# Optimization experiments

Hardware: AMD Instinct MI355X
Metric: run time of the kernel (lower is better)

## Reference

```python
import jax, jax.numpy as jnp
import numpy as np

D_MODEL = 1024
NUM_HEADS = 16
DEPTH = D_MODEL // NUM_HEADS
B, S = 2, 2048


def setup_inputs() -> dict:
    key = jax.random.key(0)
    ks = jax.random.split(key, 12)
    std = 1.0 / np.sqrt(D_MODEL)
    inp = {
        "q": jax.random.normal(ks[0], (B, S, D_MODEL), dtype=jnp.float32),
        "k": jax.random.normal(ks[1], (B, S, D_MODEL), dtype=jnp.float32),
        "v": jax.random.normal(ks[2], (B, S, D_MODEL), dtype=jnp.float32),
        "mask": jax.random.randint(ks[3], (B, 1, 1, S), 0, 2, dtype=jnp.int32),
        "wq": jax.random.normal(ks[4], (D_MODEL, D_MODEL), dtype=jnp.float32) * std,
        "bq": jnp.zeros((D_MODEL,), dtype=jnp.float32),
        "wk": jax.random.normal(ks[5], (D_MODEL, D_MODEL), dtype=jnp.float32) * std,
        "bk": jnp.zeros((D_MODEL,), dtype=jnp.float32),
        "wv": jax.random.normal(ks[6], (D_MODEL, D_MODEL), dtype=jnp.float32) * std,
        "bv": jnp.zeros((D_MODEL,), dtype=jnp.float32),
        "wo": jax.random.normal(ks[7], (D_MODEL, D_MODEL), dtype=jnp.float32) * std,
        "bo": jnp.zeros((D_MODEL,), dtype=jnp.float32),
    }
    return inp


def _split_heads(x):
    # (B, S, D) -> (B, H, S, depth)
    b, s, _ = x.shape
    return x.reshape(b, s, NUM_HEADS, DEPTH).transpose(0, 2, 1, 3)


def reference(q, k, v, mask, wq, bq, wk, bk, wv, bv, wo, bo):
    qh = _split_heads(q @ wq + bq)   # (B,H,S,depth)
    kh = _split_heads(k @ wk + bk)
    vh = _split_heads(v @ wv + bv)
    scale = 1.0 / jnp.sqrt(jnp.float32(DEPTH))
    logits = jnp.einsum("bhqd,bhkd->bhqk", qh, kh) * scale  # (B,H,Sq,Sk)
    logits = logits + mask.astype(logits.dtype) * -1e9
    attn = jax.nn.softmax(logits, axis=-1)
    out = jnp.einsum("bhqk,bhkd->bhqd", attn, vh)  # (B,H,Sq,depth)
    out = out.transpose(0, 2, 1, 3).reshape(q.shape[0], -1, D_MODEL)
    return out @ wo + bo
```

## Files before the change

kernel.cpp:

```cpp
#include <hip/hip_runtime.h>
#include <hip/hip_bf16.h>
#include <stdint.h>


typedef __bf16 bf16;
typedef __bf16 bf16x8 __attribute__((ext_vector_type(8)));
typedef __bf16 bf16x4 __attribute__((ext_vector_type(4)));
typedef float  f32x4  __attribute__((ext_vector_type(4)));

#define D_MODEL 1024
#define S_LEN   2048
#define NH      16
#define DEPTH   64

#define LOG2E   1.4426950408889634f
#define QSCALE  (0.125f * LOG2E)
#define SMAX    20.0f
#define PADPEN  (-30000.0f)

__device__ __forceinline__ void gload_lds16(const void* g, void* l) {
  __builtin_amdgcn_global_load_lds(
      (__attribute__((address_space(1))) void*)g,
      (__attribute__((address_space(3))) void*)l,
      16, 0, 0);
}

__global__ __launch_bounds__(256) void setup(
    const void* __restrict__ q, const void* __restrict__ k,
    const void* __restrict__ v, const int* __restrict__ mask,
    const void* __restrict__ wq, const void* __restrict__ wk,
    const void* __restrict__ wv, const void* __restrict__ wo,
    const void* __restrict__ bq, const void* __restrict__ bk,
    const void* __restrict__ bv, const void* __restrict__ bo,
    bf16* __restrict__ wqT, bf16* __restrict__ wkT,
    bf16* __restrict__ wvT, bf16* __restrict__ woT,
    bf16* __restrict__ bqb, bf16* __restrict__ bkb,
    bf16* __restrict__ bvb, bf16* __restrict__ bob,
    bf16* __restrict__ qb, bf16* __restrict__ kb, bf16* __restrict__ vb,
    int* __restrict__ cpos, int* __restrict__ nb, int* __restrict__ flagout)
{
  const int t = threadIdx.x;
  uint32_t w = ((const uint32_t*)q)[t];
  uint32_t e = (w >> 7) & 0xFF;
  int inr = (e >= 90 && e <= 150) ? 1 : 0;
  __shared__ int flg;
  int cnt = __syncthreads_count(inr);
  if (t == 0) flg = (cnt > 160) ? 1 : 0;
  __syncthreads();
  int flag = flg;

  const int bid = blockIdx.x;
  if (bid < 2) {
    const int b = bid;
    const int lane = t & 63, wv4 = t >> 6;
    __shared__ int wsum[4];
    int vals[8], s = 0;
#pragma unroll
    for (int j = 0; j < 8; ++j) {
      vals[j] = (mask[b * S_LEN + t * 8 + j] == 0) ? 1 : 0;
      s += vals[j];
    }
    int acc = s;
    for (int off = 1; off < 64; off <<= 1) {
      int u = __shfl_up(acc, off);
      if (lane >= off) acc += u;
    }
    if (lane == 63) wsum[wv4] = acc;
    __syncthreads();
    int base = 0;
    for (int w4 = 0; w4 < 4; ++w4) base += (w4 < wv4) ? wsum[w4] : 0;
    int ex = base + acc - s;
#pragma unroll
    for (int j = 0; j < 8; ++j) {
      cpos[b * S_LEN + t * 8 + j] = vals[j] ? ex : -1;
      ex += vals[j];
    }
    if (t == 255) nb[b] = base + acc;
    if (b == 0 && t == 0) *flagout = flag;
  } else if (bid < 6) {
    const int j = bid - 2;
    const void* B; bf16* O;
    switch (j) {
      case 0:  B = bq; O = bqb; break;
      case 1:  B = bk; O = bkb; break;
      case 2:  B = bv; O = bvb; break;
      default: B = bo; O = bob; break;
    }
    const float sc = (j == 0) ? QSCALE : 1.0f;
    for (int jj = 0; jj < 4; ++jj) {
      const int i = t + jj * 256;
      const float val = flag ? (float)((const bf16*)B)[i] : ((const float*)B)[i];
      O[i] = (bf16)(val * sc);
    }
  } else if (bid < 6 + 4096) {
    const int job = bid - 6;
    const int wsel = job >> 10, rem = job & 1023;
    const void* W; bf16* T;
    switch (wsel) {
      case 0:  W = wq; T = wqT; break;
      case 1:  W = wk; T = wkT; break;
      case 2:  W = wv; T = wvT; break;
      default: W = wo; T = woT; break;
    }
    const float sc = (wsel == 0) ? QSCALE : 1.0f;
    __shared__ float tile[32][33];
    const int tx = t & 31, ty = t >> 5;
    const int x0 = (rem & 31) * 32;
    const int y0 = (rem >> 5) * 32;
    for (int i = ty; i < 32; i += 8) {
      const size_t gi = (size_t)(y0 + i) * D_MODEL + x0 + tx;
      tile[i][tx] = flag ? (float)((const bf16*)W)[gi] : ((const float*)W)[gi];
    }
    __syncthreads();
    for (int i = ty; i < 32; i += 8)
      T[(size_t)(x0 + i) * D_MODEL + y0 + tx] = (bf16)(tile[tx][i] * sc);
  } else {
    if (flag) return;
    const int job = bid - 4102;
    const int tensor = job >> 11, blk = job & 2047;
    const void* src; bf16* dst;
    switch (tensor) {
      case 0:  src = q; dst = qb; break;
      case 1:  src = k; dst = kb; break;
      default: src = v; dst = vb; break;
    }
    const size_t idx = ((size_t)blk * 256 + t) * 8;
    const float* s = (const float*)src + idx;
    f32x4 a = *(const f32x4*)(s);
    f32x4 b2 = *(const f32x4*)(s + 4);
    bf16x8 o;
    for (int i = 0; i < 4; ++i) { o[i] = (bf16)a[i]; o[4 + i] = (bf16)b2[i]; }
    *(bf16x8*)(dst + idx) = o;
  }
}

struct GArgs {
  const bf16* A;
  const void* Araw;
  const bf16* BT;
  const bf16* bias;
  void* out;
  const int* cpos;
  int mode;
};

__device__ __forceinline__ void gemm_body(const GArgs& g, int flag)
{
  const bf16* A = flag ? (const bf16*)g.Araw : g.A;

  __shared__ __align__(16) bf16 As[128 * 32];
  __shared__ __align__(16) bf16 Bs[128 * 32];
  const int tid  = threadIdx.x;
  const int wave = tid >> 6, lane = tid & 63;
  const int quad = lane >> 4, l16 = lane & 15;

  const int flat = blockIdx.y * 8 + blockIdx.x;
  const int xcd = flat & 7, pos = flat >> 3;
  const int bx = (xcd & 1) * 4 + (pos & 3);
  const int by = (xcd >> 1) * 8 + (pos >> 2);
  const int m0 = by * 128, n0 = bx * 128;

  const int wm = (wave >> 1) * 64, wn = (wave & 1) * 64;
  const int srow = lane >> 2;
  const int scol = (lane & 3) * 8;

  f32x4 acc[4][4] = {};

  const bf16* Ag = A    + (size_t)(m0 + wave * 32 + srow) * D_MODEL + scol;
  const bf16* Bg = g.BT + (size_t)(n0 + wave * 32 + srow) * D_MODEL + scol;
  bf16* Asw = As + (wave * 32) * 32;
  bf16* Bsw = Bs + (wave * 32) * 32;

  for (int kt = 0; kt < D_MODEL; kt += 32) {
    __syncthreads();
    gload_lds16(Ag + kt,                Asw);
    gload_lds16(Ag + kt + 16 * D_MODEL, Asw + 16 * 32);
    gload_lds16(Bg + kt,                Bsw);
    gload_lds16(Bg + kt + 16 * D_MODEL, Bsw + 16 * 32);
    __syncthreads();

    bf16x8 af[4], bfv[4];
#pragma unroll
    for (int mi = 0; mi < 4; ++mi)
      af[mi] = *(const bf16x8*)(As + (wm + mi * 16 + l16) * 32 + quad * 8);
#pragma unroll
    for (int ni = 0; ni < 4; ++ni)
      bfv[ni] = *(const bf16x8*)(Bs + (wn + ni * 16 + l16) * 32 + quad * 8);
#pragma unroll
    for (int mi = 0; mi < 4; ++mi)
#pragma unroll
      for (int ni = 0; ni < 4; ++ni)
        acc[mi][ni] = __builtin_amdgcn_mfma_f32_16x16x32_bf16(
            af[mi], bfv[ni], acc[mi][ni], 0, 0, 0);
  }

#pragma unroll
  for (int mi = 0; mi < 4; ++mi) {
    const int row0 = m0 + wm + mi * 16 + quad * 4;
    const int b = row0 >> 11, s = row0 & 2047;
    int cp[4];
    if (g.mode >= 2) {
#pragma unroll
      for (int r = 0; r < 4; ++r) cp[r] = g.cpos[b * S_LEN + s + r];
    }
#pragma unroll
    for (int ni = 0; ni < 4; ++ni) {
      const int col  = n0 + wn + ni * 16 + l16;
      const float bv = (float)g.bias[col];
      const int hh = col >> 6, d = col & 63;
      if (g.mode == 3) {
        bf16* base = (bf16*)g.out + (size_t)(b * NH + hh) * S_LEN * DEPTH + d;
#pragma unroll
        for (int r = 0; r < 4; ++r)
          if (cp[r] >= 0) base[(size_t)cp[r] * DEPTH] = (bf16)(acc[mi][ni][r] + bv);
      } else if (g.mode == 2) {
        bf16* base = (bf16*)g.out + ((size_t)(b * NH + hh) * DEPTH + d) * S_LEN;
#pragma unroll
        for (int r = 0; r < 4; ++r)
          if (cp[r] >= 0) base[cp[r]] = (bf16)(acc[mi][ni][r] + bv);
      } else if (g.mode == 1) {
        bf16* op = (bf16*)g.out + ((size_t)(b * NH + hh) * S_LEN + s) * DEPTH + d;
#pragma unroll
        for (int r = 0; r < 4; ++r)
          op[(size_t)r * DEPTH] = (bf16)(acc[mi][ni][r] + bv);
      } else {
        if (flag) {
          bf16* op = (bf16*)g.out + (size_t)row0 * D_MODEL + col;
#pragma unroll
          for (int r = 0; r < 4; ++r)
            op[(size_t)r * D_MODEL] = (bf16)(acc[mi][ni][r] + bv);
        } else {
          float* op = (float*)g.out + (size_t)row0 * D_MODEL + col;
#pragma unroll
          for (int r = 0; r < 4; ++r)
            op[(size_t)r * D_MODEL] = acc[mi][ni][r] + bv;
        }
      }
    }
  }
}

__global__ __launch_bounds__(256) void gemm_qkv(GArgs g0, GArgs g1, GArgs g2,
                                                const int* __restrict__ flagp)
{
  const GArgs& g = (blockIdx.z == 0) ? g0 : ((blockIdx.z == 1) ? g1 : g2);
  gemm_body(g, *flagp);
}

__global__ __launch_bounds__(256) void gemm_out(GArgs g,
                                                const int* __restrict__ flagp)
{
  gemm_body(g, *flagp);
}

__global__ __launch_bounds__(256) void attn(
    const bf16* __restrict__ Qh, const bf16* __restrict__ Kc,
    const bf16* __restrict__ Vc, const int* __restrict__ nbp,
    bf16* __restrict__ Oh)
{
  const int bh = blockIdx.y;
  const int b  = bh >> 4;
  const int h  = bh & 15;
  const int q0 = blockIdx.x * 128;
  const int tid = threadIdx.x, wave = tid >> 6, lane = tid & 63;
  const int quad = lane >> 4, l16 = lane & 15;

  __shared__ __align__(16) bf16 Ks[64][72];
  __shared__ __align__(16) bf16 Vts[64][72];
  __shared__ __align__(16) bf16 Ps[4][32][72];

  const int nbv = nbp[b];
  const int nb_pad = (nbv + 63) & ~63;

  const bf16* Qg = Qh + ((size_t)bh * S_LEN + q0 + wave * 32) * DEPTH;
  bf16x8 aq00 = *(const bf16x8*)(Qg + (size_t)l16 * DEPTH + quad * 8);
  bf16x8 aq01 = *(const bf16x8*)(Qg + (size_t)l16 * DEPTH + 32 + quad * 8);
  bf16x8 aq10 = *(const bf16x8*)(Qg + (size_t)(16 + l16) * DEPTH + quad * 8);
  bf16x8 aq11 = *(const bf16x8*)(Qg + (size_t)(16 + l16) * DEPTH + 32 + quad * 8);

  bf16x8 ones;
#pragma unroll
  for (int j = 0; j < 8; ++j) ones[j] = (bf16)1.0f;

  f32x4 o_acc[2][4] = {};
  f32x4 l_acc[2] = {};

  const bf16* Kg = Kc + (size_t)bh * S_LEN * DEPTH;
  const bf16* Vg = Vc + (size_t)bh * DEPTH * S_LEN;

  const int sr0 = tid >> 3, sc0 = (tid & 7) * 8;
  const int sr1 = sr0 + 32;

  bf16x8 kr0, kr1, vr0, vr1;
  {
    kr0 = *(const bf16x8*)(Kg + (size_t)sr0 * DEPTH + sc0);
    kr1 = *(const bf16x8*)(Kg + (size_t)sr1 * DEPTH + sc0);
    vr0 = *(const bf16x8*)(Vg + (size_t)sr0 * S_LEN + sc0);
    vr1 = *(const bf16x8*)(Vg + (size_t)sr1 * S_LEN + sc0);
  }

  for (int kb = 0; kb < nb_pad; kb += 64) {
    __syncthreads();
    *(bf16x8*)(&Ks[sr0][sc0])  = kr0;
    *(bf16x8*)(&Ks[sr1][sc0])  = kr1;
    *(bf16x8*)(&Vts[sr0][sc0]) = vr0;
    *(bf16x8*)(&Vts[sr1][sc0]) = vr1;
    __syncthreads();
    if (kb + 64 < nb_pad) {
      kr0 = *(const bf16x8*)(Kg + (size_t)(kb + 64 + sr0) * DEPTH + sc0);
      kr1 = *(const bf16x8*)(Kg + (size_t)(kb + 64 + sr1) * DEPTH + sc0);
      vr0 = *(const bf16x8*)(Vg + (size_t)sr0 * S_LEN + kb + 64 + sc0);
      vr1 = *(const bf16x8*)(Vg + (size_t)sr1 * S_LEN + kb + 64 + sc0);
    }

    f32x4 sacc[2][4] = {};
#pragma unroll
    for (int jn = 0; jn < 4; ++jn) {
      bf16x8 bk0 = *(const bf16x8*)(&Ks[jn * 16 + l16][quad * 8]);
      bf16x8 bk1 = *(const bf16x8*)(&Ks[jn * 16 + l16][32 + quad * 8]);
      sacc[0][jn] = __builtin_amdgcn_mfma_f32_16x16x32_bf16(aq00, bk0, sacc[0][jn], 0, 0, 0);
      sacc[0][jn] = __builtin_amdgcn_mfma_f32_16x16x32_bf16(aq01, bk1, sacc[0][jn], 0, 0, 0);
      sacc[1][jn] = __builtin_amdgcn_mfma_f32_16x16x32_bf16(aq10, bk0, sacc[1][jn], 0, 0, 0);
      sacc[1][jn] = __builtin_amdgcn_mfma_f32_16x16x32_bf16(aq11, bk1, sacc[1][jn], 0, 0, 0);
    }

#pragma unroll
    for (int jn = 0; jn < 4; ++jn) {
      const int key = kb + jn * 16 + l16;
      const float pen = (key < nbv) ? (-SMAX) : PADPEN;
#pragma unroll
      for (int qs = 0; qs < 2; ++qs)
#pragma unroll
        for (int r = 0; r < 4; ++r)
          Ps[wave][qs * 16 + quad * 4 + r][jn * 16 + l16] =
              (bf16)__builtin_amdgcn_exp2f(sacc[qs][jn][r] + pen);
    }

    bf16x8 ap00 = *(const bf16x8*)(&Ps[wave][l16][quad * 8]);
    bf16x8 ap01 = *(const bf16x8*)(&Ps[wave][l16][32 + quad * 8]);
    bf16x8 ap10 = *(const bf16x8*)(&Ps[wave][16 + l16][quad * 8]);
    bf16x8 ap11 = *(const bf16x8*)(&Ps[wave][16 + l16][32 + quad * 8]);
#pragma unroll
    for (int jd = 0; jd < 4; ++jd) {
      bf16x8 bv0 = *(const bf16x8*)(&Vts[jd * 16 + l16][quad * 8]);
      bf16x8 bv1 = *(const bf16x8*)(&Vts[jd * 16 + l16][32 + quad * 8]);
      o_acc[0][jd] = __builtin_amdgcn_mfma_f32_16x16x32_bf16(ap00, bv0, o_acc[0][jd], 0, 0, 0);
      o_acc[0][jd] = __builtin_amdgcn_mfma_f32_16x16x32_bf16(ap01, bv1, o_acc[0][jd], 0, 0, 0);
      o_acc[1][jd] = __builtin_amdgcn_mfma_f32_16x16x32_bf16(ap10, bv0, o_acc[1][jd], 0, 0, 0);
      o_acc[1][jd] = __builtin_amdgcn_mfma_f32_16x16x32_bf16(ap11, bv1, o_acc[1][jd], 0, 0, 0);
    }
    l_acc[0] = __builtin_amdgcn_mfma_f32_16x16x32_bf16(ap00, ones, l_acc[0], 0, 0, 0);
    l_acc[0] = __builtin_amdgcn_mfma_f32_16x16x32_bf16(ap01, ones, l_acc[0], 0, 0, 0);
    l_acc[1] = __builtin_amdgcn_mfma_f32_16x16x32_bf16(ap10, ones, l_acc[1], 0, 0, 0);
    l_acc[1] = __builtin_amdgcn_mfma_f32_16x16x32_bf16(ap11, ones, l_acc[1], 0, 0, 0);
  }

#pragma unroll
  for (int qs = 0; qs < 2; ++qs) {
#pragma unroll
    for (int r = 0; r < 4; ++r) {
      const int s = q0 + wave * 32 + qs * 16 + quad * 4 + r;
      const float inv = 1.f / l_acc[qs][r];
#pragma unroll
      for (int jd = 0; jd < 4; ++jd) {
        const int d = jd * 16 + l16;
        Oh[(size_t)(b * S_LEN + s) * D_MODEL + h * DEPTH + d] =
            (bf16)(o_acc[qs][jd][r] * inv);
      }
    }
  }
}

extern "C" void kernel_launch(void* const* d_in, const int* in_sizes, int n_in,
                              void* d_out, int out_size, void* d_ws, size_t ws_size,
                              hipStream_t stream)
{
  const void* q    = d_in[0];
  const void* k    = d_in[1];
  const void* v    = d_in[2];
  const int*  mask = (const int*)d_in[3];
  const void* wq   = d_in[4];
  const void* bq   = d_in[5];
  const void* wk   = d_in[6];
  const void* bk   = d_in[7];
  const void* wv   = d_in[8];
  const void* bv   = d_in[9];
  const void* wo   = d_in[10];
  const void* bo   = d_in[11];

  char* ws = (char*)d_ws;
  const size_t MB = 1u << 20;
  bf16* Qh  = (bf16*)(ws + 0 * MB);
  bf16* Kc  = (bf16*)(ws + 8 * MB);
  bf16* Vc  = (bf16*)(ws + 16 * MB);
  bf16* Oh  = (bf16*)(ws + 24 * MB);
  bf16* wqT = (bf16*)(ws + 32 * MB);
  bf16* wkT = (bf16*)(ws + 34 * MB);
  bf16* wvT = (bf16*)(ws + 36 * MB);
  bf16* woT = (bf16*)(ws + 38 * MB);
  bf16* bqb = (bf16*)(ws + 40 * MB);
  bf16* bkb = (bf16*)(ws + 40 * MB + 4096);
  bf16* bvb = (bf16*)(ws + 40 * MB + 8192);
  bf16* bob = (bf16*)(ws + 40 * MB + 12288);
  int*  flag = (int*)(ws + 40 * MB + 32768);
  int*  cpos = (int*)(ws + 40 * MB + 65536);
  int*  nb   = (int*)(ws + 40 * MB + 65536 + 16384);
  bf16* qb  = (bf16*)(ws + 41 * MB);
  bf16* kb_ = (bf16*)(ws + 49 * MB);
  bf16* vb_ = (bf16*)(ws + 57 * MB);

  setup<<<10246, 256, 0, stream>>>(
      q, k, v, mask, wq, wk, wv, wo, bq, bk, bv, bo,
      wqT, wkT, wvT, woT, bqb, bkb, bvb, bob,
      qb, kb_, vb_, cpos, nb, flag);

  GArgs gq{qb,  q,  wqT, bqb, Qh, nullptr, 1};
  GArgs gk{kb_, k,  wkT, bkb, Kc, cpos,    3};
  GArgs gv{vb_, v,  wvT, bvb, Vc, cpos,    2};
  gemm_qkv<<<dim3(8, 32, 3), 256, 0, stream>>>(gq, gk, gv, flag);

  attn<<<dim3(16, 32), 256, 0, stream>>>(Qh, Kc, Vc, nb, Oh);

  GArgs go{Oh, Oh, woT, bob, d_out, nullptr, 0};
  gemm_out<<<dim3(8, 32), 256, 0, stream>>>(go, flag);
}
```

Baseline: 229.8 us.

## Gather unmasked rows into K/V projection GEMM and double-buffer LDS tiles

Setup now builds a compacted list of unmasked key positions per batch instead of a scatter map. The K and V projection GEMMs gather only those rows, skip whole 128-row tiles past the padded count, and write results contiguously, which removes roughly half the K/V GEMM work under the random mask. The GEMM main loop also gains two LDS buffers so the next tile's loads overlap the current tile's MFMAs, and the XCD-aware block swizzle is dropped. Both the doubled LDS footprint and the loss of the swizzle could lower occupancy or L2 locality.

```diff
diff --git a/kernel.cpp b/kernel.cpp
--- a/kernel.cpp
+++ b/kernel.cpp
@@ -37,7 +37,7 @@
     bf16* __restrict__ bqb, bf16* __restrict__ bkb,
     bf16* __restrict__ bvb, bf16* __restrict__ bob,
     bf16* __restrict__ qb, bf16* __restrict__ kb, bf16* __restrict__ vb,
-    int* __restrict__ cpos, int* __restrict__ nb, int* __restrict__ flagout)
+    int* __restrict__ rlist, int* __restrict__ nb, int* __restrict__ flagout)
 {
   const int t = threadIdx.x;
   uint32_t w = ((const uint32_t*)q)[t];
@@ -72,10 +72,14 @@
     int ex = base + acc - s;
 #pragma unroll
     for (int j = 0; j < 8; ++j) {
-      cpos[b * S_LEN + t * 8 + j] = vals[j] ? ex : -1;
-      ex += vals[j];
-    }
-    if (t == 255) nb[b] = base + acc;
+      if (vals[j]) { rlist[b * S_LEN + ex] = t * 8 + j; ex += 1; }
+    }
+    const int total = wsum[0] + wsum[1] + wsum[2] + wsum[3];
+    if (t < 128) {
+      const int idx = total + t;
+      if (idx < S_LEN) rlist[b * S_LEN + idx] = 0;
+    }
+    if (t == 0) nb[b] = total;
     if (b == 0 && t == 0) *flagout = flag;
   } else if (bid < 6) {
     const int j = bid - 2;
@@ -140,86 +144,104 @@
   const bf16* BT;
   const bf16* bias;
   void* out;
-  const int* cpos;
+  const int* rlist;
+  const int* nb;
   int mode;
 };
 
 __device__ __forceinline__ void gemm_body(const GArgs& g, int flag)
 {
   const bf16* A = flag ? (const bf16*)g.Araw : g.A;
-
-  __shared__ __align__(16) bf16 As[128 * 32];
-  __shared__ __align__(16) bf16 Bs[128 * 32];
   const int tid  = threadIdx.x;
   const int wave = tid >> 6, lane = tid & 63;
   const int quad = lane >> 4, l16 = lane & 15;
-
-  const int flat = blockIdx.y * 8 + blockIdx.x;
-  const int xcd = flat & 7, pos = flat >> 3;
-  const int bx = (xcd & 1) * 4 + (pos & 3);
-  const int by = (xcd >> 1) * 8 + (pos >> 2);
-  const int m0 = by * 128, n0 = bx * 128;
+  const int m0 = blockIdx.y * 128, n0 = blockIdx.x * 128;
+  const int b = m0 >> 11, j0 = m0 & 2047;
+
+  if (g.mode >= 2) {
+    const int nbp = (g.nb[b] + 127) & ~127;
+    if (j0 >= nbp) return;
+  }
 
   const int wm = (wave >> 1) * 64, wn = (wave & 1) * 64;
   const int srow = lane >> 2;
   const int scol = (lane & 3) * 8;
 
+  size_t ar0, ar1;
+  if (g.mode >= 2) {
+    ar0 = (size_t)b * S_LEN + g.rlist[b * S_LEN + j0 + wave * 32 + srow];
+    ar1 = (size_t)b * S_LEN + g.rlist[b * S_LEN + j0 + wave * 32 + 16 + srow];
+  } else {
+    ar0 = (size_t)m0 + wave * 32 + srow;
+    ar1 = ar0 + 16;
+  }
+  const bf16* Ag0 = A + ar0 * D_MODEL + scol;
+  const bf16* Ag1 = A + ar1 * D_MODEL + scol;
+  const bf16* Bg  = g.BT + (size_t)(n0 + wave * 32 + srow) * D_MODEL + scol;
+
+  __shared__ __align__(16) bf16 As[2][128 * 32];
+  __shared__ __align__(16) bf16 Bs[2][128 * 32];
+  bf16* Aw0 = As[0] + (wave * 32) * 32;
+  bf16* Aw1 = As[1] + (wave * 32) * 32;
+  bf16* Bw0 = Bs[0] + (wave * 32) * 32;
+  bf16* Bw1 = Bs[1] + (wave * 32) * 32;
+
   f32x4 acc[4][4] = {};
 
-  const bf16* Ag = A    + (size_t)(m0 + wave * 32 + srow) * D_MODEL + scol;
-  const bf16* Bg = g.BT + (size_t)(n0 + wave * 32 + srow) * D_MODEL + scol;
-  bf16* Asw = As + (wave * 32) * 32;
-  bf16* Bsw = Bs + (wave * 32) * 32;
-
-  for (int kt = 0; kt < D_MODEL; kt += 32) {
-    __syncthreads();
-    gload_lds16(Ag + kt,                Asw);
-    gload_lds16(Ag + kt + 16 * D_MODEL, Asw + 16 * 32);
-    gload_lds16(Bg + kt,                Bsw);
-    gload_lds16(Bg + kt + 16 * D_MODEL, Bsw + 16 * 32);
-    __syncthreads();
-
+  auto stage = [&](int buf, int kt) {
+    bf16* Aw = buf ? Aw1 : Aw0;
+    bf16* Bw = buf ? Bw1 : Bw0;
+    gload_lds16(Ag0 + kt, Aw);
+    gload_lds16(Ag1 + kt, Aw + 16 * 32);
+    gload_lds16(Bg  + kt, Bw);
+    gload_lds16(Bg + kt + 16 * D_MODEL, Bw + 16 * 32);
+  };
+  auto compute = [&](int buf) {
+    const bf16* Ab = As[buf];
+    const bf16* Bb = Bs[buf];
     bf16x8 af[4], bfv[4];
 #pragma unroll
     for (int mi = 0; mi < 4; ++mi)
-      af[mi] = *(const bf16x8*)(As + (wm + mi * 16 + l16) * 32 + quad * 8);
+      af[mi] = *(const bf16x8*)(Ab + (wm + mi * 16 + l16) * 32 + quad * 8);
 #pragma unroll
     for (int ni = 0; ni < 4; ++ni)
-      bfv[ni] = *(const bf16x8*)(Bs + (wn + ni * 16 + l16) * 32 + quad * 8);
+      bfv[ni] = *(const bf16x8*)(Bb + (wn + ni * 16 + l16) * 32 + quad * 8);
 #pragma unroll
     for (int mi = 0; mi < 4; ++mi)
 #pragma unroll
       for (int ni = 0; ni < 4; ++ni)
         acc[mi][ni] = __builtin_amdgcn_mfma_f32_16x16x32_bf16(
             af[mi], bfv[ni], acc[mi][ni], 0, 0, 0);
+  };
+
+  stage(0, 0);
+#pragma unroll 1
+  for (int kt = 0; kt < D_MODEL; kt += 64) {
+    __syncthreads();
+    if (kt + 32 < D_MODEL) stage(1, kt + 32);
+    compute(0);
+    __syncthreads();
+    if (kt + 64 < D_MODEL) stage(0, kt + 64);
+    compute(1);
   }
 
 #pragma unroll
   for (int mi = 0; mi < 4; ++mi) {
     const int row0 = m0 + wm + mi * 16 + quad * 4;
-    const int b = row0 >> 11, s = row0 & 2047;
-    int cp[4];
-    if (g.mode >= 2) {
-#pragma unroll
-      for (int r = 0; r < 4; ++r) cp[r] = g.cpos[b * S_LEN + s + r];
-    }
+    const int rj = row0 & 2047;
 #pragma unroll
     for (int ni = 0; ni < 4; ++ni) {
       const int col  = n0 + wn + ni * 16 + l16;
       const float bv = (float)g.bias[col];
       const int hh = col >> 6, d = col & 63;
-      if (g.mode == 3) {
-        bf16* base = (bf16*)g.out + (size_t)(b * NH + hh) * S_LEN * DEPTH + d;
-#pragma unroll
-        for (int r = 0; r < 4; ++r)
-          if (cp[r] >= 0) base[(size_t)cp[r] * DEPTH] = (bf16)(acc[mi][ni][r] + bv);
-      } else if (g.mode == 2) {
-        bf16* base = (bf16*)g.out + ((size_t)(b * NH + hh) * DEPTH + d) * S_LEN;
-#pragma unroll
-        for (int r = 0; r < 4; ++r)
-          if (cp[r] >= 0) base[cp[r]] = (bf16)(acc[mi][ni][r] + bv);
-      } else if (g.mode == 1) {
-        bf16* op = (bf16*)g.out + ((size_t)(b * NH + hh) * S_LEN + s) * DEPTH + d;
+      if (g.mode == 2) {
+        bf16x4 pk;
+#pragma unroll
+        for (int r = 0; r < 4; ++r) pk[r] = (bf16)(acc[mi][ni][r] + bv);
+        *(bf16x4*)((bf16*)g.out +
+                   ((size_t)(b * NH + hh) * DEPTH + d) * S_LEN + rj) = pk;
+      } else if (g.mode == 1 || g.mode == 3) {
+        bf16* op = (bf16*)g.out + ((size_t)(b * NH + hh) * S_LEN + rj) * DEPTH + d;
 #pragma unroll
         for (int r = 0; r < 4; ++r)
           op[(size_t)r * DEPTH] = (bf16)(acc[mi][ni][r] + bv);
@@ -292,12 +314,10 @@
   const int sr1 = sr0 + 32;
 
   bf16x8 kr0, kr1, vr0, vr1;
-  {
-    kr0 = *(const bf16x8*)(Kg + (size_t)sr0 * DEPTH + sc0);
-    kr1 = *(const bf16x8*)(Kg + (size_t)sr1 * DEPTH + sc0);
-    vr0 = *(const bf16x8*)(Vg + (size_t)sr0 * S_LEN + sc0);
-    vr1 = *(const bf16x8*)(Vg + (size_t)sr1 * S_LEN + sc0);
-  }
+  kr0 = *(const bf16x8*)(Kg + (size_t)sr0 * DEPTH + sc0);
+  kr1 = *(const bf16x8*)(Kg + (size_t)sr1 * DEPTH + sc0);
+  vr0 = *(const bf16x8*)(Vg + (size_t)sr0 * S_LEN + sc0);
+  vr1 = *(const bf16x8*)(Vg + (size_t)sr1 * S_LEN + sc0);
 
   for (int kb = 0; kb < nb_pad; kb += 64) {
     __syncthreads();
@@ -403,7 +423,7 @@
   bf16* bvb = (bf16*)(ws + 40 * MB + 8192);
   bf16* bob = (bf16*)(ws + 40 * MB + 12288);
   int*  flag = (int*)(ws + 40 * MB + 32768);
-  int*  cpos = (int*)(ws + 40 * MB + 65536);
+  int*  rlist = (int*)(ws + 40 * MB + 65536);
   int*  nb   = (int*)(ws + 40 * MB + 65536 + 16384);
   bf16* qb  = (bf16*)(ws + 41 * MB);
   bf16* kb_ = (bf16*)(ws + 49 * MB);
@@ -412,15 +432,15 @@
   setup<<<10246, 256, 0, stream>>>(
       q, k, v, mask, wq, wk, wv, wo, bq, bk, bv, bo,
       wqT, wkT, wvT, woT, bqb, bkb, bvb, bob,
-      qb, kb_, vb_, cpos, nb, flag);
-
-  GArgs gq{qb,  q,  wqT, bqb, Qh, nullptr, 1};
-  GArgs gk{kb_, k,  wkT, bkb, Kc, cpos,    3};
-  GArgs gv{vb_, v,  wvT, bvb, Vc, cpos,    2};
+      qb, kb_, vb_, rlist, nb, flag);
+
+  GArgs gq{qb,  q,  wqT, bqb, Qh, nullptr, nullptr, 1};
+  GArgs gk{kb_, k,  wkT, bkb, Kc, rlist,   nb,      3};
+  GArgs gv{vb_, v,  wvT, bvb, Vc, rlist,   nb,      2};
   gemm_qkv<<<dim3(8, 32, 3), 256, 0, stream>>>(gq, gk, gv, flag);
 
   attn<<<dim3(16, 32), 256, 0, stream>>>(Qh, Kc, Vc, nb, Oh);
 
-  GArgs go{Oh, Oh, woT, bob, d_out, nullptr, 0};
+  GArgs go{Oh, Oh, woT, bob, d_out, nullptr, nullptr, 0};
   gemm_out<<<dim3(8, 32), 256, 0, stream>>>(go, flag);
 }
```

New measurement: 239.8 us. +4.4%, slower.
